# Kernel tuning notes

Hardware: AMD Instinct MI355X
Metric: run time of the kernel (lower is better)

The kernel has to match this reference:

```python
import jax, jax.numpy as jnp
import numpy as np

# ---- static config (matches init_kwargs) ----
N, E = 8192, 262144
IN_CH, MP_CH, HID, K = 128, 512, 256, 10
EPS, DELTA = 1e-3, 0.311
TV_COEFF, BAL_COEFF = 0.785, 0.514


def setup_inputs() -> dict:
    key = jax.random.key(0)
    ks = jax.random.split(key, 16)

    def p(k, shape):
        fan_in = shape[0] if len(shape) > 1 else shape[0]
        return (jax.random.normal(k, shape, jnp.float32) / np.sqrt(fan_in)).astype(jnp.float32)

    return {
        "x": jax.random.normal(ks[0], (N, IN_CH), jnp.float32),
        "edge_index": jax.random.randint(ks[1], (2, E), 0, N, jnp.int32),
        "edge_weight": jax.random.uniform(ks[2], (E,), jnp.float32),
        # GTVConv layer 1 / 2 (Linear weight + bias)
        "W1": p(ks[3], (IN_CH, MP_CH)), "b1": jnp.zeros((MP_CH,), jnp.float32),
        "W2": p(ks[4], (MP_CH, MP_CH)), "b2": jnp.zeros((MP_CH,), jnp.float32),
        # pooling MLP [512 -> 256 -> K], relu, no norm
        "Wm1": p(ks[5], (MP_CH, HID)), "bm1": jnp.zeros((HID,), jnp.float32),
        "Wm2": p(ks[6], (HID, K)), "bm2": jnp.zeros((K,), jnp.float32),
    }


def _gtv_conv(x, src, dst, w, W, b):
    """GTVConv: out = elu( h - delta*(D_G h - Gamma h) + b ),
    gamma_ij = w_ij / max(||h_i - h_j||_1, eps), h = x @ W."""
    h = x @ W                                   # [N, C]
    diff = jnp.sum(jnp.abs(h[src] - h[dst]), axis=-1)   # [E]
    gamma = w / jnp.maximum(diff, EPS)                  # [E]
    deg = jnp.zeros(h.shape[0], h.dtype).at[dst].add(gamma)          # [N]
    agg = jnp.zeros_like(h).at[dst].add(gamma[:, None] * h[src])     # Gamma @ h
    out = h - DELTA * (deg[:, None] * h - agg) + b
    return jax.nn.elu(out)


def reference(x, edge_index, edge_weight, W1, b1, W2, b2, Wm1, bm1, Wm2, bm2):
    src, dst = edge_index[0], edge_index[1]

    h = _gtv_conv(x, src, dst, edge_weight, W1, b1)
    h = _gtv_conv(h, src, dst, edge_weight, W2, b2)

    # pooling MLP -> cluster logits s
    s_logits = jax.nn.relu(h @ Wm1 + bm1) @ Wm2 + bm2   # [N, K]

    # dense adjacency (to_dense_adj: duplicate edges accumulate)
    adj = jnp.zeros((N, N), x.dtype).at[src, dst].add(edge_weight)

    s = jax.nn.softmax(s_logits, axis=-1)

    # total-variation loss: sum_ij a_ij * sum_k |s_ik - s_jk| / (2 * nnz(adj))
    tv = jnp.zeros((), x.dtype)
    for k in range(K):  # small fixed loop over clusters, avoids [N,N,K] tensor
        col = s[:, k]
        tv = tv + jnp.sum(adj * jnp.abs(col[:, None] - col[None, :]))
    n_edges = jax.lax.stop_gradient(jnp.count_nonzero(adj).astype(x.dtype))
    tv = tv / (2.0 * n_edges)

    # asymmetric-norm balance loss (AsymCheegerCut)
    idx = N // K + 1                         # rho-quantile index (static)
    quant = jnp.sort(s, axis=0)[N - idx]     # idx-th largest per cluster, [K]
    t = s - quant[None, :]
    asym = jnp.where(t >= 0, (K - 1) * t, -t)
    denom = float(N * (K - 1))
    bal = (denom - jnp.sum(asym)) / denom

    return s_logits, TV_COEFF * tv, BAL_COEFF * bal
```

## Files before the change

### kernel.cpp

```cpp
#include <hip/hip_runtime.h>

#define N_NODES 8192
#define N_EDGES 262144
#define IN_CH 128
#define MP_CH 512
#define HID 256
#define KCL 10
#define EPS_C 0.001f
#define DELTA_C 0.311f
#define TV_COEFF_C 0.785f
#define BAL_COEFF_C 0.514f
#define RANK1 7373
#define DBINS 80


typedef __bf16 bf16x8 __attribute__((ext_vector_type(8)));
typedef float f32x4 __attribute__((ext_vector_type(4)));
typedef unsigned short ushort8 __attribute__((ext_vector_type(8)));

__device__ __forceinline__ float bf2f(unsigned short h) {
  union { unsigned int u; float f; } c; c.u = ((unsigned int)h) << 16; return c.f;
}
__device__ __forceinline__ unsigned short f2bf(float f) {
  union { float f; unsigned int u; } c; c.f = f;
  unsigned int r = c.u + 0x7fffu + ((c.u >> 16) & 1u);
  return (unsigned short)(r >> 16);
}

__global__ void prep_kernel(const float* __restrict__ x, const float* __restrict__ W1,
                            const float* __restrict__ W2, const float* __restrict__ Wm1,
                            unsigned short* __restrict__ xb, unsigned short* __restrict__ W1bt,
                            unsigned short* __restrict__ W2bt, unsigned short* __restrict__ Wm1bt,
                            const int* __restrict__ dst, int* __restrict__ cnt) {
  int i = blockIdx.x * 256 + threadIdx.x;
  if (i < 1048576) { xb[i] = f2bf(x[i]); return; }
  i -= 1048576;
  if (i < 65536) { int n = i >> 7, k = i & 127; W1bt[i] = f2bf(W1[k * MP_CH + n]); return; }
  i -= 65536;
  if (i < 262144) { int n = i >> 9, k = i & 511; W2bt[i] = f2bf(W2[k * MP_CH + n]); return; }
  i -= 262144;
  if (i < 131072) { int n = i >> 9, k = i & 511; Wm1bt[i] = f2bf(Wm1[k * HID + n]); return; }
  i -= 131072;
  if (i < N_EDGES) atomicAdd(&cnt[dst[i]], 1);
}

__global__ __launch_bounds__(256) void gemm1_scan(
    const unsigned short* __restrict__ A, const unsigned short* __restrict__ BT,
    unsigned short* __restrict__ Cb, const int* __restrict__ cnt, int* __restrict__ offs,
    int* __restrict__ cursor, int* __restrict__ nodeorder) {
  if (blockIdx.x < 256) {
    __shared__ unsigned short lsm[2 * 128 * 32];
    unsigned short* lA = lsm;
    unsigned short* lB = lsm + 128 * 32;
    const int N = MP_CH, K = IN_CH;
    int lane = threadIdx.x & 63;
    int wv = threadIdx.x >> 6;
    int tm = (blockIdx.x >> 2) * 128, tn = (blockIdx.x & 3) * 128;
    int wm = (wv >> 1) * 64, wn = (wv & 1) * 64;
    int rA = lane & 15, quad = lane >> 4;
    f32x4 acc[4][4];
#pragma unroll
    for (int i = 0; i < 4; ++i)
#pragma unroll
      for (int j = 0; j < 4; ++j) acc[i][j] = (f32x4){0.f, 0.f, 0.f, 0.f};
    int arow = wv * 32 + (lane >> 2);
    int acol = (lane & 3) * 8;
    for (int k0 = 0; k0 < K; k0 += 32) {
#pragma unroll
      for (int c = 0; c < 2; ++c) {
        const unsigned short* ga = A + (size_t)(tm + arow + c * 16) * K + k0 + acol;
        __builtin_amdgcn_global_load_lds(
            (const __attribute__((address_space(1))) unsigned int*)ga,
            (__attribute__((address_space(3))) unsigned int*)(lA + (wv * 32 + c * 16) * 32),
            16, 0, 0);
        const unsigned short* gb = BT + (size_t)(tn + arow + c * 16) * K + k0 + acol;
        __builtin_amdgcn_global_load_lds(
            (const __attribute__((address_space(1))) unsigned int*)gb,
            (__attribute__((address_space(3))) unsigned int*)(lB + (wv * 32 + c * 16) * 32),
            16, 0, 0);
      }
      __syncthreads();
      bf16x8 af[4], bfr[4];
#pragma unroll
      for (int i = 0; i < 4; ++i)
        af[i] = *(const bf16x8*)(lA + (wm + i * 16 + rA) * 32 + quad * 8);
#pragma unroll
      for (int j = 0; j < 4; ++j)
        bfr[j] = *(const bf16x8*)(lB + (wn + j * 16 + rA) * 32 + quad * 8);
#pragma unroll
      for (int i = 0; i < 4; ++i)
#pragma unroll
        for (int j = 0; j < 4; ++j)
          acc[i][j] = __builtin_amdgcn_mfma_f32_16x16x32_bf16(af[i], bfr[j], acc[i][j], 0, 0, 0);
      __syncthreads();
    }
    float* fbuf = (float*)lsm;
    int band = threadIdx.x >> 7;
    int rrow = (threadIdx.x >> 3) & 15;
    int cg = threadIdx.x & 7;
#pragma unroll
    for (int i = 0; i < 4; ++i) {
#pragma unroll
      for (int j = 0; j < 4; ++j)
#pragma unroll
        for (int r = 0; r < 4; ++r)
          fbuf[(wv >> 1) * (16 * 128) + (quad * 4 + r) * 128 + (wn + j * 16 + rA)] =
              acc[i][j][r];
      __syncthreads();
      const float* sr = fbuf + band * (16 * 128) + rrow * 128 + cg * 16;
      unsigned short ov[16];
#pragma unroll
      for (int c = 0; c < 16; ++c) ov[c] = f2bf(sr[c]);
      size_t gbase = (size_t)(tm + band * 64 + i * 16 + rrow) * N + tn + cg * 16;
      *(ushort8*)(Cb + gbase) = *(ushort8*)ov;
      *(ushort8*)(Cb + gbase + 8) = *(ushort8*)(ov + 8);
      __syncthreads();
    }
  } else {
    __shared__ int ts[256];
    __shared__ int dh[DBINS];
    int t = threadIdx.x;
    int v[32]; int ssum = 0;
#pragma unroll
    for (int j = 0; j < 32; ++j) { v[j] = cnt[t * 32 + j]; ssum += v[j]; }
    if (t < DBINS) dh[t] = 0;
    ts[t] = ssum; __syncthreads();
    for (int off = 1; off < 256; off <<= 1) {
      int add = (t >= off) ? ts[t - off] : 0;
      __syncthreads();
      ts[t] += add;
      __syncthreads();
    }
    int base = ts[t] - ssum;
#pragma unroll
    for (int j = 0; j < 32; ++j) {
      offs[t * 32 + j] = base; cursor[t * 32 + j] = base; base += v[j];
      int key = v[j] < (DBINS - 1) ? v[j] : (DBINS - 1);
      atomicAdd(&dh[(DBINS - 1) - key], 1);
    }
    if (t == 255) offs[N_NODES] = ts[255];
    __syncthreads();
    if (t == 0) {
      int acc0 = 0;
      for (int b = 0; b < DBINS; ++b) { int c = dh[b]; dh[b] = acc0; acc0 += c; }
    }
    __syncthreads();
#pragma unroll
    for (int j = 0; j < 32; ++j) {
      int key = v[j] < (DBINS - 1) ? v[j] : (DBINS - 1);
      int pos = atomicAdd(&dh[(DBINS - 1) - key], 1);
      nodeorder[pos] = t * 32 + j;
    }
  }
}

__global__ void fill_kernel(const int* __restrict__ src, const int* __restrict__ dst,
                            const float* __restrict__ ew, int* __restrict__ cursor,
                            int2* __restrict__ esw) {
  for (int e = blockIdx.x * blockDim.x + threadIdx.x; e < N_EDGES; e += gridDim.x * blockDim.x) {
    int p = atomicAdd(&cursor[dst[e]], 1);
    esw[p] = make_int2(src[e], __float_as_int(ew[e]));
  }
}

__global__ __launch_bounds__(256) void gemm_bt(
    const unsigned short* __restrict__ A, const unsigned short* __restrict__ BT,
    unsigned short* __restrict__ Cb, int N, int K) {
  __shared__ unsigned short lsm[2 * 128 * 32];
  unsigned short* lA = lsm;
  unsigned short* lB = lsm + 128 * 32;
  int lane = threadIdx.x & 63;
  int wv = threadIdx.x >> 6;
  int tm = blockIdx.y * 128, tn = blockIdx.x * 128;
  int wm = (wv >> 1) * 64, wn = (wv & 1) * 64;
  int rA = lane & 15, quad = lane >> 4;
  f32x4 acc[4][4];
#pragma unroll
  for (int i = 0; i < 4; ++i)
#pragma unroll
    for (int j = 0; j < 4; ++j) acc[i][j] = (f32x4){0.f, 0.f, 0.f, 0.f};

  int arow = wv * 32 + (lane >> 2);
  int acol = (lane & 3) * 8;

  for (int k0 = 0; k0 < K; k0 += 32) {
#pragma unroll
    for (int c = 0; c < 2; ++c) {
      const unsigned short* ga = A + (size_t)(tm + arow + c * 16) * K + k0 + acol;
      __builtin_amdgcn_global_load_lds(
          (const __attribute__((address_space(1))) unsigned int*)ga,
          (__attribute__((address_space(3))) unsigned int*)(lA + (wv * 32 + c * 16) * 32),
          16, 0, 0);
      const unsigned short* gb = BT + (size_t)(tn + arow + c * 16) * K + k0 + acol;
      __builtin_amdgcn_global_load_lds(
          (const __attribute__((address_space(1))) unsigned int*)gb,
          (__attribute__((address_space(3))) unsigned int*)(lB + (wv * 32 + c * 16) * 32),
          16, 0, 0);
    }
    __syncthreads();
    bf16x8 af[4], bfr[4];
#pragma unroll
    for (int i = 0; i < 4; ++i)
      af[i] = *(const bf16x8*)(lA + (wm + i * 16 + rA) * 32 + quad * 8);
#pragma unroll
    for (int j = 0; j < 4; ++j)
      bfr[j] = *(const bf16x8*)(lB + (wn + j * 16 + rA) * 32 + quad * 8);
#pragma unroll
    for (int i = 0; i < 4; ++i)
#pragma unroll
      for (int j = 0; j < 4; ++j)
        acc[i][j] = __builtin_amdgcn_mfma_f32_16x16x32_bf16(af[i], bfr[j], acc[i][j], 0, 0, 0);
    __syncthreads();
  }

  float* fbuf = (float*)lsm;
  int band = threadIdx.x >> 7;
  int rrow = (threadIdx.x >> 3) & 15;
  int cg = threadIdx.x & 7;
#pragma unroll
  for (int i = 0; i < 4; ++i) {
#pragma unroll
    for (int j = 0; j < 4; ++j)
#pragma unroll
      for (int r = 0; r < 4; ++r)
        fbuf[(wv >> 1) * (16 * 128) + (quad * 4 + r) * 128 + (wn + j * 16 + rA)] =
            acc[i][j][r];
    __syncthreads();
    const float* sr = fbuf + band * (16 * 128) + rrow * 128 + cg * 16;
    unsigned short ov[16];
#pragma unroll
    for (int c = 0; c < 16; ++c) ov[c] = f2bf(sr[c]);
    size_t gbase = (size_t)(tm + band * 64 + i * 16 + rrow) * N + tn + cg * 16;
    *(ushort8*)(Cb + gbase) = *(ushort8*)ov;
    *(ushort8*)(Cb + gbase + 8) = *(ushort8*)(ov + 8);
    __syncthreads();
  }
}

__global__ __launch_bounds__(256, 8) void gtv_node(
    const unsigned short* __restrict__ hb, const float* __restrict__ bias,
    const int2* __restrict__ esw, const int* __restrict__ offs,
    const int* __restrict__ nodeorder, unsigned short* __restrict__ outb) {
  __shared__ float sacc[2][MP_CH];
  int lane = threadIdx.x & 63;
  int wv = threadIdx.x >> 6;
  int pair = wv >> 1;
  int half = wv & 1;
  int d = __builtin_amdgcn_readfirstlane(nodeorder[blockIdx.x * 2 + pair]);
  ushort8 hdv = ((const ushort8*)(hb + (size_t)d * MP_CH))[lane];
  float hd[8], acc[8];
#pragma unroll
  for (int j = 0; j < 8; ++j) { hd[j] = bf2f(hdv[j]); acc[j] = 0.f; }
  int n0 = offs[d], n1 = offs[d + 1];
  int mid = n0 + ((n1 - n0 + 1) >> 1);
  int e0 = half ? mid : n0;
  int e1 = half ? n1 : mid;
  int i = e0;
  for (; i + 1 < e1; i += 2) {
    int2 ma = esw[i], mb = esw[i + 1];
    float wa = __int_as_float(ma.y), wb = __int_as_float(mb.y);
    ushort8 va = ((const ushort8*)(hb + (size_t)ma.x * MP_CH))[lane];
    ushort8 vb = ((const ushort8*)(hb + (size_t)mb.x * MP_CH))[lane];
    float pa = 0.f, pb = 0.f;
#pragma unroll
    for (int j = 0; j < 8; ++j) {
      pa += fabsf(hd[j] - bf2f(va[j]));
      pb += fabsf(hd[j] - bf2f(vb[j]));
    }
#pragma unroll
    for (int m = 1; m < 64; m <<= 1) { pa += __shfl_xor(pa, m, 64); pb += __shfl_xor(pb, m, 64); }
    float ga = wa * __builtin_amdgcn_rcpf(fmaxf(pa, EPS_C));
    float gb = wb * __builtin_amdgcn_rcpf(fmaxf(pb, EPS_C));
#pragma unroll
    for (int j = 0; j < 8; ++j)
      acc[j] += ga * (hd[j] - bf2f(va[j])) + gb * (hd[j] - bf2f(vb[j]));
  }
  if (i < e1) {
    int2 m0 = esw[i];
    float w = __int_as_float(m0.y);
    ushort8 sv = ((const ushort8*)(hb + (size_t)m0.x * MP_CH))[lane];
    float part = 0.f;
#pragma unroll
    for (int j = 0; j < 8; ++j) part += fabsf(hd[j] - bf2f(sv[j]));
#pragma unroll
    for (int m = 1; m < 64; m <<= 1) part += __shfl_xor(part, m, 64);
    float g = w * __builtin_amdgcn_rcpf(fmaxf(part, EPS_C));
#pragma unroll
    for (int j = 0; j < 8; ++j) acc[j] += g * (hd[j] - bf2f(sv[j]));
  }
  if (half) {
#pragma unroll
    for (int j = 0; j < 8; ++j) sacc[pair][lane * 8 + j] = acc[j];
  }
  __syncthreads();
  if (!half) {
    const f32x4* br = (const f32x4*)(bias + lane * 8);
    f32x4 b0 = br[0], b1 = br[1];
    unsigned short ov[8];
#pragma unroll
    for (int j = 0; j < 8; ++j) {
      float tot = acc[j] + sacc[pair][lane * 8 + j];
      float bv = (j < 4) ? b0[j] : b1[j - 4];
      float o = hd[j] - DELTA_C * tot + bv;
      o = (o > 0.f) ? o : (expf(o) - 1.f);
      ov[j] = f2bf(o);
    }
    *((ushort8*)(outb + (size_t)d * MP_CH) + lane) = *(ushort8*)ov;
  }
}

__global__ __launch_bounds__(256) void head_fused(
    const unsigned short* __restrict__ A,
    const unsigned short* __restrict__ BT,
    const float* __restrict__ bm1v, const float* __restrict__ Wm2v,
    const float* __restrict__ bm2v, float* __restrict__ out, float* __restrict__ s) {
  __shared__ unsigned short lA[32 * 32];
  __shared__ unsigned short lB[256 * 32];
  __shared__ float hbuf[256 * 41];
  __shared__ float lW2[HID * KCL];
  __shared__ float lb1[HID];
  __shared__ float lb2[KCL];
  int t = threadIdx.x;
  int lane = t & 63, wv = t >> 6;
  int rA = lane & 15, quad = lane >> 4;
  int m0 = blockIdx.x * 32;

  for (int i2 = t; i2 < HID * KCL; i2 += 256) lW2[i2] = Wm2v[i2];
  lb1[t < HID ? t : 0] = bm1v[t < HID ? t : 0];
  if (t < KCL) lb2[t] = bm2v[t];

  f32x4 acc[2][4];
#pragma unroll
  for (int i = 0; i < 2; ++i)
#pragma unroll
    for (int j = 0; j < 4; ++j) acc[i][j] = (f32x4){0.f, 0.f, 0.f, 0.f};

  for (int k0 = 0; k0 < MP_CH; k0 += 32) {
    if (wv < 2) {
      int row = wv * 16 + (lane >> 2);
      const unsigned short* ga = A + (size_t)(m0 + row) * MP_CH + k0 + (lane & 3) * 8;
      __builtin_amdgcn_global_load_lds(
          (const __attribute__((address_space(1))) unsigned int*)ga,
          (__attribute__((address_space(3))) unsigned int*)(lA + (wv * 16) * 32), 16, 0, 0);
    }
#pragma unroll
    for (int q = 0; q < 4; ++q) {
      int idx = wv * 4 + q;
      int row = idx * 16 + (lane >> 2);
      const unsigned short* gb = BT + (size_t)row * MP_CH + k0 + (lane & 3) * 8;
      __builtin_amdgcn_global_load_lds(
          (const __attribute__((address_space(1))) unsigned int*)gb,
          (__attribute__((address_space(3))) unsigned int*)(lB + (idx * 16) * 32), 16, 0, 0);
    }
    __syncthreads();
    bf16x8 af[2], bfr[4];
#pragma unroll
    for (int i = 0; i < 2; ++i)
      af[i] = *(const bf16x8*)(lA + (i * 16 + rA) * 32 + quad * 8);
#pragma unroll
    for (int j = 0; j < 4; ++j)
      bfr[j] = *(const bf16x8*)(lB + (wv * 64 + j * 16 + rA) * 32 + quad * 8);
#pragma unroll
    for (int i = 0; i < 2; ++i)
#pragma unroll
      for (int j = 0; j < 4; ++j)
        acc[i][j] = __builtin_amdgcn_mfma_f32_16x16x32_bf16(af[i], bfr[j], acc[i][j], 0, 0, 0);
    __syncthreads();
  }

#pragma unroll
  for (int i = 0; i < 2; ++i)
#pragma unroll
    for (int j = 0; j < 4; ++j)
#pragma unroll
      for (int r = 0; r < 4; ++r) {
        int row = i * 16 + quad * 4 + r;
        int col = wv * 64 + j * 16 + rA;
        hbuf[col * 41 + row] = fmaxf(acc[i][j][r] + lb1[col], 0.f);
      }
  __syncthreads();

  int row = t >> 3, g = t & 7;
  float p[KCL];
#pragma unroll
  for (int n = 0; n < KCL; ++n) p[n] = 0.f;
#pragma unroll
  for (int k = 0; k < 32; ++k) {
    int col = k * 8 + g;
    float hv = hbuf[col * 41 + row];
    const float* wr = lW2 + col * KCL;
#pragma unroll
    for (int n = 0; n < KCL; ++n) p[n] += hv * wr[n];
  }
#pragma unroll
  for (int n = 0; n < KCL; ++n) {
    p[n] += __shfl_xor(p[n], 1, 64);
    p[n] += __shfl_xor(p[n], 2, 64);
    p[n] += __shfl_xor(p[n], 4, 64);
  }
  if (g == 0) {
    float vv[KCL]; float mx = -1e30f;
    size_t gr = (size_t)(m0 + row);
#pragma unroll
    for (int n = 0; n < KCL; ++n) {
      vv[n] = p[n] + lb2[n];
      out[gr * KCL + n] = vv[n];
      mx = fmaxf(mx, vv[n]);
    }
    float sum = 0.f;
#pragma unroll
    for (int n = 0; n < KCL; ++n) { vv[n] = expf(vv[n] - mx); sum += vv[n]; }
    float inv = 1.f / sum;
#pragma unroll
    for (int n = 0; n < KCL; ++n) s[gr * KCL + n] = vv[n] * inv;
  }
}

__global__ __launch_bounds__(1024) void tvquant_kernel(
    const int* __restrict__ src, const int* __restrict__ dst,
    const float* __restrict__ ew, const float* __restrict__ s,
    unsigned int* __restrict__ bitmap, float* __restrict__ scal) {
  __shared__ float fsh[16];
  __shared__ int wcnt[2][16];
  int t = threadIdx.x;
  int lane = t & 63, wv = t >> 6;
  if (blockIdx.x < 246) {
    float local = 0.f;
    for (int e = blockIdx.x * 1024 + t; e < N_EDGES; e += 246 * 1024) {
      int a = src[e], b = dst[e];
      float w = ew[e];
      const float* sa = s + (size_t)a * KCL;
      const float* sb = s + (size_t)b * KCL;
      float tv = 0.f;
#pragma unroll
      for (int k = 0; k < KCL; ++k) tv += fabsf(sa[k] - sb[k]);
      local += w * tv;
      if (w != 0.f) {
        unsigned int key = ((unsigned int)a << 13) | (unsigned int)b;
        atomicOr(&bitmap[key >> 5], 1u << (key & 31u));
      }
    }
#pragma unroll
    for (int m = 1; m < 64; m <<= 1) local += __shfl_xor(local, m, 64);
    if (lane == 0) fsh[wv] = local;
    __syncthreads();
    if (t == 0) {
      float tot = 0.f;
#pragma unroll
      for (int i2 = 0; i2 < 16; ++i2) tot += fsh[i2];
      atomicAdd(&scal[0], tot);
    }
  } else {
    int k = blockIdx.x - 246;
    unsigned int v[8];
#pragma unroll
    for (int j = 0; j < 8; ++j)
      v[j] = __float_as_uint(s[(size_t)(t + j * 1024) * KCL + k]);
    unsigned int lo = 0u, hi = 0x3F800000u;
    int p = 0;
    while (lo < hi) {
      unsigned int mid = (lo + hi) >> 1;
      int c = 0;
#pragma unroll
      for (int j = 0; j < 8; ++j) c += (v[j] <= mid) ? 1 : 0;
#pragma unroll
      for (int m = 1; m < 64; m <<= 1) c += __shfl_xor(c, m, 64);
      if (lane == 0) wcnt[p][wv] = c;
      __syncthreads();
      int tot = 0;
#pragma unroll
      for (int i2 = 0; i2 < 16; ++i2) tot += wcnt[p][i2];
      if (tot >= RANK1) hi = mid; else lo = mid + 1;
      p ^= 1;
    }
    float q = __uint_as_float(lo);
    float local = 0.f;
#pragma unroll
    for (int j = 0; j < 8; ++j) {
      float tt = __uint_as_float(v[j]) - q;
      local += (tt >= 0.f) ? 9.f * tt : -tt;
    }
#pragma unroll
    for (int m = 1; m < 64; m <<= 1) local += __shfl_xor(local, m, 64);
    if (lane == 0) fsh[wv] = local;
    __syncthreads();
    if (t == 0) {
      float tot = 0.f;
#pragma unroll
      for (int i2 = 0; i2 < 16; ++i2) tot += fsh[i2];
      atomicAdd(&scal[1], tot);
    }
  }
}

__global__ __launch_bounds__(1024) void popcfin_kernel(const unsigned int* __restrict__ bm,
                                                       float* __restrict__ scal,
                                                       float* __restrict__ out) {
  __shared__ int ish[16];
  int t = threadIdx.x;
  int lane = t & 63, wv = t >> 6;
  int local = 0;
  for (int i = blockIdx.x * 1024 + t; i < (1 << 21); i += 256 * 1024)
    local += __popc(bm[i]);
#pragma unroll
  for (int m = 1; m < 64; m <<= 1) local += __shfl_xor(local, m, 64);
  if (lane == 0) ish[wv] = local;
  __syncthreads();
  if (t == 0) {
    int tot = 0;
#pragma unroll
    for (int i2 = 0; i2 < 16; ++i2) tot += ish[i2];
    atomicAdd((int*)(scal + 2), tot);
    __threadfence();
    int d = atomicAdd((int*)(scal + 3), 1);
    if (d == 255) {
      float tv = scal[0], asym = scal[1];
      float nedges = (float)(*(int*)(scal + 2));
      out[N_NODES * KCL] = TV_COEFF_C * (tv / (2.f * nedges));
      out[N_NODES * KCL + 1] = BAL_COEFF_C * ((73728.f - asym) / 73728.f);
    }
  }
}

#define OFF_BM     ((size_t)0)
#define OFF_CNT    ((size_t)8388608)
#define OFF_SCAL   ((size_t)8421376)
#define OFF_OFFS   ((size_t)8421888)
#define OFF_CURSOR ((size_t)8454912)
#define OFF_NORD   ((size_t)8487936)
#define OFF_HB     ((size_t)16777216)
#define OFF_OUTB   ((size_t)25165824)
#define OFF_ESW    ((size_t)33554432)
#define OFF_XB     ((size_t)41943040)
#define OFF_W1BT   ((size_t)44040192)
#define OFF_W2BT   ((size_t)44171264)
#define OFF_WM1BT  ((size_t)44695552)
#define OFF_S      ((size_t)44957696)

extern "C" void kernel_launch(void* const* d_in, const int* in_sizes, int n_in,
                              void* d_out, int out_size, void* d_ws, size_t ws_size,
                              hipStream_t stream) {
  const float* x   = (const float*)d_in[0];
  const int*   ei  = (const int*)d_in[1];
  const float* ew  = (const float*)d_in[2];
  const float* W1  = (const float*)d_in[3];
  const float* b1  = (const float*)d_in[4];
  const float* W2  = (const float*)d_in[5];
  const float* b2  = (const float*)d_in[6];
  const float* Wm1 = (const float*)d_in[7];
  const float* bm1 = (const float*)d_in[8];
  const float* Wm2 = (const float*)d_in[9];
  const float* bm2 = (const float*)d_in[10];
  float* out = (float*)d_out;

  char* ws = (char*)d_ws;
  unsigned int*   bitmap = (unsigned int*)(ws + OFF_BM);
  int*            cnt    = (int*)(ws + OFF_CNT);
  float*          scal   = (float*)(ws + OFF_SCAL);
  int*            offs   = (int*)(ws + OFF_OFFS);
  int*            cursor = (int*)(ws + OFF_CURSOR);
  int*            nord   = (int*)(ws + OFF_NORD);
  unsigned short* hb     = (unsigned short*)(ws + OFF_HB);
  unsigned short* outb   = (unsigned short*)(ws + OFF_OUTB);
  int2*           esw    = (int2*)(ws + OFF_ESW);
  unsigned short* xb     = (unsigned short*)(ws + OFF_XB);
  unsigned short* W1bt   = (unsigned short*)(ws + OFF_W1BT);
  unsigned short* W2bt   = (unsigned short*)(ws + OFF_W2BT);
  unsigned short* Wm1bt  = (unsigned short*)(ws + OFF_WM1BT);
  float*          s      = (float*)(ws + OFF_S);

  const int* srcA = ei;
  const int* dstA = ei + N_EDGES;

  hipMemsetAsync(ws, 0, 8421632, stream);

  prep_kernel<<<6912, 256, 0, stream>>>(x, W1, W2, Wm1, xb, W1bt, W2bt, Wm1bt, dstA, cnt);
  gemm1_scan<<<257, 256, 0, stream>>>(xb, W1bt, hb, cnt, offs, cursor, nord);
  fill_kernel<<<1024, 256, 0, stream>>>(srcA, dstA, ew, cursor, esw);

  gtv_node<<<N_NODES / 2, 256, 0, stream>>>(hb, b1, esw, offs, nord, outb);
  gemm_bt<<<dim3(MP_CH / 128, N_NODES / 128), 256, 0, stream>>>(outb, W2bt, hb, MP_CH, MP_CH);
  gtv_node<<<N_NODES / 2, 256, 0, stream>>>(hb, b2, esw, offs, nord, outb);
  head_fused<<<N_NODES / 32, 256, 0, stream>>>(outb, Wm1bt, bm1, Wm2, bm2, out, s);

  tvquant_kernel<<<256, 1024, 0, stream>>>(srcA, dstA, ew, s, bitmap, scal);
  popcfin_kernel<<<256, 1024, 0, stream>>>(bitmap, scal, out);
}
```

Baseline: 247.9 us.

## Count distinct adjacency entries from CSR segments instead of a dense bitmap

Drops the 8 MB dense N×N bitmap, its memset, the atomicOr per edge, and the popcount kernel. Distinct nonzero (src,dst) pairs are now counted per destination segment of the CSR edge list, using wave shuffles plus an LDS staging buffer for duplicate detection. The final scalar computation moves into the last tvquant block. This saves the large memset and scan traffic but adds an O(deg²) duplicate check per node. Offset changes also leave some workspace regions unaligned.

```diff
diff --git a/kernel.cpp b/kernel.cpp
--- a/kernel.cpp
+++ b/kernel.cpp
@@ -163,6 +163,53 @@
   }
 }
 
+__global__ __launch_bounds__(1024) void dupcount_kernel(const int2* __restrict__ esw,
+                                                        const int* __restrict__ offs,
+                                                        float* __restrict__ scal) {
+  __shared__ int lsrc[16][320];
+  __shared__ int csh[16];
+  int t = threadIdx.x;
+  int lane = t & 63, wv = t >> 6;
+  int c = 0;
+#pragma unroll
+  for (int nn = 0; nn < 2; ++nn) {
+    int d = (blockIdx.x * 16 + wv) * 2 + nn;
+    int n0 = offs[d], n1 = offs[d + 1];
+    for (int bse = n0; bse < n1; bse += 64) {
+      int e = bse + lane;
+      int2 me = (e < n1) ? esw[e] : make_int2(-1, 0);
+      bool act = (e < n1) && (me.y != 0);
+      bool dup = false;
+      unsigned long long am = __ballot(act);
+      for (int ofs = 1; ofs < 64; ++ofs) {
+        int ol = lane - ofs;
+        int osrc = __shfl(me.x, (lane + 64 - ofs) & 63, 64);
+        if (act && ol >= 0 && ((am >> ol) & 1ull) && osrc == me.x) dup = true;
+      }
+      int idx0 = bse - n0;
+      int staged = idx0 < 320 ? idx0 : 320;
+      for (int j = 0; j < staged; ++j) {
+        if (act && lsrc[wv][j] == me.x) dup = true;
+      }
+      for (int j = n0 + 320; j < bse; ++j) {
+        int2 ej = esw[j];
+        if (act && ej.y != 0 && ej.x == me.x) dup = true;
+      }
+      unsigned long long b = __ballot(act && !dup);
+      if (lane == 0) c += __popcll(b);
+      if (idx0 + lane < 320) lsrc[wv][idx0 + lane] = act ? me.x : -1;
+    }
+  }
+  if (lane == 0) csh[wv] = c;
+  __syncthreads();
+  if (t == 0) {
+    int tot = 0;
+#pragma unroll
+    for (int i = 0; i < 16; ++i) tot += csh[i];
+    if (tot) atomicAdd((int*)(scal + 2), tot);
+  }
+}
+
 __global__ __launch_bounds__(256) void gemm_bt(
     const unsigned short* __restrict__ A, const unsigned short* __restrict__ BT,
     unsigned short* __restrict__ Cb, int N, int K) {
@@ -419,7 +466,7 @@
 __global__ __launch_bounds__(1024) void tvquant_kernel(
     const int* __restrict__ src, const int* __restrict__ dst,
     const float* __restrict__ ew, const float* __restrict__ s,
-    unsigned int* __restrict__ bitmap, float* __restrict__ scal) {
+    float* __restrict__ scal, float* __restrict__ out) {
   __shared__ float fsh[16];
   __shared__ int wcnt[2][16];
   int t = threadIdx.x;
@@ -435,10 +482,6 @@
 #pragma unroll
       for (int k = 0; k < KCL; ++k) tv += fabsf(sa[k] - sb[k]);
       local += w * tv;
-      if (w != 0.f) {
-        unsigned int key = ((unsigned int)a << 13) | (unsigned int)b;
-        atomicOr(&bitmap[key >> 5], 1u << (key & 31u));
-      }
     }
 #pragma unroll
     for (int m = 1; m < 64; m <<= 1) local += __shfl_xor(local, m, 64);
@@ -491,43 +534,24 @@
       atomicAdd(&scal[1], tot);
     }
   }
-}
-
-__global__ __launch_bounds__(1024) void popcfin_kernel(const unsigned int* __restrict__ bm,
-                                                       float* __restrict__ scal,
-                                                       float* __restrict__ out) {
-  __shared__ int ish[16];
-  int t = threadIdx.x;
-  int lane = t & 63, wv = t >> 6;
-  int local = 0;
-  for (int i = blockIdx.x * 1024 + t; i < (1 << 21); i += 256 * 1024)
-    local += __popc(bm[i]);
-#pragma unroll
-  for (int m = 1; m < 64; m <<= 1) local += __shfl_xor(local, m, 64);
-  if (lane == 0) ish[wv] = local;
-  __syncthreads();
   if (t == 0) {
-    int tot = 0;
-#pragma unroll
-    for (int i2 = 0; i2 < 16; ++i2) tot += ish[i2];
-    atomicAdd((int*)(scal + 2), tot);
     __threadfence();
-    int d = atomicAdd((int*)(scal + 3), 1);
-    if (d == 255) {
-      float tv = scal[0], asym = scal[1];
-      float nedges = (float)(*(int*)(scal + 2));
-      out[N_NODES * KCL] = TV_COEFF_C * (tv / (2.f * nedges));
+    int dn = atomicAdd((int*)(scal + 3), 1);
+    if (dn == 255) {
+      float tv = atomicAdd(&scal[0], 0.f);
+      float asym = atomicAdd(&scal[1], 0.f);
+      int ne = atomicAdd((int*)(scal + 2), 0);
+      out[N_NODES * KCL] = TV_COEFF_C * (tv / (2.f * (float)ne));
       out[N_NODES * KCL + 1] = BAL_COEFF_C * ((73728.f - asym) / 73728.f);
     }
   }
 }
 
-#define OFF_BM     ((size_t)0)
-#define OFF_CNT    ((size_t)8388608)
-#define OFF_SCAL   ((size_t)8421376)
-#define OFF_OFFS   ((size_t)8421888)
-#define OFF_CURSOR ((size_t)8454912)
-#define OFF_NORD   ((size_t)8487936)
+#define OFF_CNT    ((size_t)0)
+#define OFF_SCAL   ((size_t)32768)
+#define OFF_OFFS   ((size_t)33024)
+#define OFF_CURSOR ((size_t)65796)
+#define OFF_NORD   ((size_t)98564)
 #define OFF_HB     ((size_t)16777216)
 #define OFF_OUTB   ((size_t)25165824)
 #define OFF_ESW    ((size_t)33554432)
@@ -554,7 +578,6 @@
   float* out = (float*)d_out;
 
   char* ws = (char*)d_ws;
-  unsigned int*   bitmap = (unsigned int*)(ws + OFF_BM);
   int*            cnt    = (int*)(ws + OFF_CNT);
   float*          scal   = (float*)(ws + OFF_SCAL);
   int*            offs   = (int*)(ws + OFF_OFFS);
@@ -572,17 +595,17 @@
   const int* srcA = ei;
   const int* dstA = ei + N_EDGES;
 
-  hipMemsetAsync(ws, 0, 8421632, stream);
+  hipMemsetAsync(ws, 0, 33024, stream);
 
   prep_kernel<<<6912, 256, 0, stream>>>(x, W1, W2, Wm1, xb, W1bt, W2bt, Wm1bt, dstA, cnt);
   gemm1_scan<<<257, 256, 0, stream>>>(xb, W1bt, hb, cnt, offs, cursor, nord);
   fill_kernel<<<1024, 256, 0, stream>>>(srcA, dstA, ew, cursor, esw);
+  dupcount_kernel<<<256, 1024, 0, stream>>>(esw, offs, scal);
 
   gtv_node<<<N_NODES / 2, 256, 0, stream>>>(hb, b1, esw, offs, nord, outb);
   gemm_bt<<<dim3(MP_CH / 128, N_NODES / 128), 256, 0, stream>>>(outb, W2bt, hb, MP_CH, MP_CH);
   gtv_node<<<N_NODES / 2, 256, 0, stream>>>(hb, b2, esw, offs, nord, outb);
   head_fused<<<N_NODES / 32, 256, 0, stream>>>(outb, Wm1bt, bm1, Wm2, bm2, out, s);
 
-  tvquant_kernel<<<256, 1024, 0, stream>>>(srcA, dstA, ew, s, bitmap, scal);
-  popcfin_kernel<<<256, 1024, 0, stream>>>(bitmap, scal, out);
-}
+  tvquant_kernel<<<256, 1024, 0, stream>>>(srcA, dstA, ew, s, scal, out);
+}
```

New measurement: 257.0 us. 1.04x slower.
